# Performance work log

Hardware: AMD Instinct MI355X
Metric: run time of the kernel (lower is better)

The kernel has to match this reference:

```python
import jax, jax.numpy as jnp
import numpy as np

H = 300          # node_hidden_dim (GINE output dim)
D = 2 * H        # set2set in_channels = 600
STEPS = 2        # num_step_set2_set


def _lstm_cell(x, h, c, W_ih, W_hh, b_ih, b_hh):
    # PyTorch LSTM gate order: i, f, g, o
    gates = x @ W_ih.T + h @ W_hh.T + b_ih + b_hh
    i, f, g, o = jnp.split(gates, 4, axis=-1)
    c = jax.nn.sigmoid(f) * c + jax.nn.sigmoid(i) * jnp.tanh(g)
    h = jax.nn.sigmoid(o) * jnp.tanh(c)
    return h, c


def _set2set(x, batch, num_graphs, W_ih, W_hh, b_ih, b_hh):
    # torch_geometric Set2Set with processing_steps=STEPS, 1-layer LSTM
    B = num_graphs
    q_star = jnp.zeros((B, 2 * D), x.dtype)
    h = jnp.zeros((B, D), x.dtype)
    c = jnp.zeros((B, D), x.dtype)
    for _ in range(STEPS):
        h, c = _lstm_cell(q_star, h, c, W_ih, W_hh, b_ih, b_hh)
        q = h                                   # [B, D]
        e = jnp.sum(x * q[batch], axis=-1)      # [N]
        emax = jax.ops.segment_max(e, batch, num_segments=B)
        a = jnp.exp(e - emax[batch])
        asum = jax.ops.segment_sum(a, batch, num_segments=B)
        a = a / (asum[batch] + 1e-16)           # segment softmax
        r = jax.ops.segment_sum(a[:, None] * x, batch, num_segments=B)
        q_star = jnp.concatenate([q, r], axis=-1)   # [B, 2D]
    return q_star


def _l2norm(x):
    return x / jnp.maximum(jnp.linalg.norm(x, axis=1, keepdims=True), 1e-12)


def setup_inputs() -> dict:
    key = jax.random.key(0)
    ks = jax.random.split(key, 8)
    Nu, Nv, B = 8192, 8192, 256
    solute_x = jax.random.normal(ks[0], (Nu, H), jnp.float32)
    solvent_x = jax.random.normal(ks[1], (Nv, H), jnp.float32)
    solute_batch = jnp.sort(jax.random.randint(ks[2], (Nu,), 0, B)).astype(jnp.int32)
    solvent_batch = jnp.sort(jax.random.randint(ks[3], (Nv,), 0, B)).astype(jnp.int32)
    lstm_W_ih = jax.random.normal(ks[4], (4 * D, 2 * D), jnp.float32) * 0.02
    lstm_W_hh = jax.random.normal(ks[5], (4 * D, D), jnp.float32) * 0.02
    lstm_b_ih = jnp.zeros((4 * D,), jnp.float32)
    lstm_b_hh = jnp.zeros((4 * D,), jnp.float32)
    pred_W = jax.random.normal(ks[6], (1, 8 * H), jnp.float32) * 0.02
    pred_b = jnp.zeros((1,), jnp.float32)
    return {
        "solute_x": solute_x, "solvent_x": solvent_x,
        "solute_batch": solute_batch, "solvent_batch": solvent_batch,
        "num_graphs": B,
        "lstm_W_ih": lstm_W_ih, "lstm_W_hh": lstm_W_hh,
        "lstm_b_ih": lstm_b_ih, "lstm_b_hh": lstm_b_hh,
        "pred_W": pred_W, "pred_b": pred_b,
    }


def reference(solute_x, solvent_x, solute_batch, solvent_batch, num_graphs,
              lstm_W_ih, lstm_W_hh, lstm_b_ih, lstm_b_hh, pred_W, pred_b):
    # F.normalize(dim=1)
    su = _l2norm(solute_x)    # [Nu, H]
    sv = _l2norm(solvent_x)   # [Nv, H]
    # len_map = solute_len.T @ solvent_len == same-pair membership mask
    mask = (solute_batch[:, None] == solvent_batch[None, :]).astype(su.dtype)
    interaction_map = (su @ sv.T) * mask          # [Nu, Nv]
    ret_interaction_map = interaction_map
    solvent_prime = interaction_map.T @ su        # [Nv, H]
    solute_prime = interaction_map @ sv           # [Nu, H]
    su2 = jnp.concatenate([su, solute_prime], axis=1)    # [Nu, 2H]
    sv2 = jnp.concatenate([sv, solvent_prime], axis=1)   # [Nv, 2H]
    su_s2s = _set2set(su2, solute_batch, num_graphs, lstm_W_ih, lstm_W_hh, lstm_b_ih, lstm_b_hh)
    sv_s2s = _set2set(sv2, solvent_batch, num_graphs, lstm_W_ih, lstm_W_hh, lstm_b_ih, lstm_b_hh)
    final = jnp.concatenate([su_s2s, sv_s2s], axis=1)    # [B, 8H]
    predictions = final @ pred_W.T + pred_b              # [B, 1]
    return predictions, ret_interaction_map
```

## Files before the change

kernel.cpp:

```cpp
#include <hip/hip_runtime.h>
#include <math.h>

#define HDIM 300
#define DDIM 600
#define NGR  256

typedef float vf4 __attribute__((ext_vector_type(4)));
typedef float vf2 __attribute__((ext_vector_type(2)));

__device__ __forceinline__ float wred_sum(float v){
  #pragma unroll
  for(int o=32;o;o>>=1) v += __shfl_xor(v,o,64);
  return v;
}
__device__ __forceinline__ float wred_max(float v){
  #pragma unroll
  for(int o=32;o;o>>=1) v = fmaxf(v,__shfl_xor(v,o,64));
  return v;
}
__device__ __forceinline__ float sigm(float x){ return 1.f/(1.f+expf(-x)); }

__global__ __launch_bounds__(256) void k_norm_fill_off(const float* __restrict__ xu,
    const float* __restrict__ xv, float* __restrict__ su, float* __restrict__ sv,
    int Nu, int Nv, const int* __restrict__ ub, const int* __restrict__ vb,
    int* __restrict__ uoff, int* __restrict__ voff,
    const float* __restrict__ b_ih, const float* __restrict__ b_hh,
    float* __restrict__ h1, float* __restrict__ c1,
    const float* __restrict__ pb, float* __restrict__ outp,
    float* __restrict__ mapbase){
  int NBn = (Nu + Nv) >> 2;
  int b = blockIdx.x;
  if (b == NBn){
    int t = threadIdx.x;
    if (t < NGR){
      int lo=0, hi=Nu;
      while(lo<hi){ int m=(lo+hi)>>1; if (ub[m] < t) lo=m+1; else hi=m; }
      uoff[t]=lo;
      lo=0; hi=Nv;
      while(lo<hi){ int m=(lo+hi)>>1; if (vb[m] < t) lo=m+1; else hi=m; }
      voff[t]=lo;
      if (t==0){ uoff[NGR]=Nu; voff[NGR]=Nv; }
      outp[t] = pb[0];
    }
    for (int d=threadIdx.x; d<DDIM; d+=256){
      float gi = b_ih[d]      + b_hh[d];
      float gg = b_ih[1200+d] + b_hh[1200+d];
      float go = b_ih[1800+d] + b_hh[1800+d];
      float c  = sigm(gi)*tanhf(gg);
      c1[d]=c; h1[d]=sigm(go)*tanhf(c);
    }
    return;
  }
  if (b > NBn){
    int i = b - NBn - 1;
    int g = ub[i];
    int lo=0, hi=Nv;
    while(lo<hi){ int m=(lo+hi)>>1; if (vb[m] < g) lo=m+1; else hi=m; }
    int js = lo;
    hi = Nv;
    while(lo<hi){ int m=(lo+hi)>>1; if (vb[m] <= g) lo=m+1; else hi=m; }
    int je = lo;
    float* mrow = mapbase + (size_t)i*Nv;
    const vf4 z4 = {0.f,0.f,0.f,0.f};
    int nf4 = Nv >> 2;
    for (int q4=threadIdx.x; q4<nf4; q4+=256){
      int j0 = q4*4;
      if (j0+4 <= js || j0 >= je){
        __builtin_nontemporal_store(z4, (vf4*)(mrow + j0));
      } else {
        #pragma unroll
        for(int u=0;u<4;u++){ int j=j0+u; if (j<js || j>=je) mrow[j]=0.f; }
      }
    }
    return;
  }
  int wid = b*4 + (threadIdx.x >> 6);
  int lane = threadIdx.x & 63;
  const float* src; float* dst;
  if (wid < Nu){ src = xu + (size_t)wid*HDIM; dst = su + (size_t)wid*HDIM; }
  else         { src = xv + (size_t)(wid-Nu)*HDIM; dst = sv + (size_t)(wid-Nu)*HDIM; }
  const vf4* s4 = (const vf4*)src;
  vf4 A = s4[lane];
  vf4 Bv = (lane<11)? s4[64+lane] : (vf4){0.f,0.f,0.f,0.f};
  float s = A.x*A.x+A.y*A.y+A.z*A.z+A.w*A.w + Bv.x*Bv.x+Bv.y*Bv.y+Bv.z*Bv.z+Bv.w*Bv.w;
  s = wred_sum(s);
  float inv = 1.f / fmaxf(sqrtf(s), 1e-12f);
  vf4* d4 = (vf4*)dst;
  d4[lane] = A*inv;
  if (lane<11) d4[64+lane] = Bv*inv;
}

__global__ __launch_bounds__(256) void k_prime(const float* __restrict__ su,
    const float* __restrict__ sv, const int* __restrict__ ub,
    const int* __restrict__ vb, const int* __restrict__ uoff,
    const int* __restrict__ voff, float* __restrict__ spr,
    float* __restrict__ svp, float* __restrict__ e1u, float* __restrict__ e1v,
    const float* __restrict__ h1, float* __restrict__ mapbase, int Nu, int Nv){
  int b = blockIdx.x;
  bool isU = (b < Nu);
  int i = isU ? b : b - Nu;
  const float* xa = isU ? su : sv;
  const float* xb = isU ? sv : su;
  const int* mybatch = isU ? ub : vb;
  const int* ooff    = isU ? voff : uoff;
  float* prime = isU ? spr : svp;
  float* eout  = isU ? e1u : e1v;

  int tid = threadIdx.x, lane = tid & 63, w = tid >> 6;
  __shared__ __align__(16) float xrow[304];
  __shared__ __align__(16) float prl[4*304];
  __shared__ float qv[2*HDIM];
  __shared__ float red[4];
  const float* rowp = xa + (size_t)i*HDIM;
  for (int t=tid; t<HDIM;   t+=256) xrow[t] = rowp[t];
  for (int t=tid; t<2*HDIM; t+=256) qv[t]   = h1[t];
  int g = mybatch[i];
  int js = ooff[g], je = ooff[g+1];
  __syncthreads();

  const vf4* x4 = (const vf4*)xrow;
  vf4 xA = x4[lane];
  vf4 xB = (lane<11)? x4[64+lane] : (vf4){0.f,0.f,0.f,0.f};
  vf4 prA = {0.f,0.f,0.f,0.f}, prB = {0.f,0.f,0.f,0.f};
  for (int j = js + w; j < je; j += 4){
    const vf4* orow = (const vf4*)(xb + (size_t)j*HDIM);
    vf4 oA = orow[lane];
    vf4 oB = (lane<11)? orow[64+lane] : (vf4){0.f,0.f,0.f,0.f};
    float d = oA.x*xA.x + oA.y*xA.y + oA.z*xA.z + oA.w*xA.w
            + oB.x*xB.x + oB.y*xB.y + oB.z*xB.z + oB.w*xB.w;
    d = wred_sum(d);
    if (isU && lane==0) mapbase[(size_t)i*Nv + j] = d;
    prA += d * oA;
    prB += d * oB;
  }
  vf4* p4 = (vf4*)(prl + w*304);
  p4[lane] = prA;
  if (lane<11) p4[64+lane] = prB;
  __syncthreads();
  float ep = 0.f;
  for (int t=tid; t<HDIM; t+=256){
    float s = prl[t] + prl[304+t] + prl[608+t] + prl[912+t];
    prime[(size_t)i*HDIM + t] = s;
    ep += xrow[t]*qv[t] + s*qv[HDIM+t];
  }
  ep = wred_sum(ep);
  if (lane==0) red[w] = ep;
  __syncthreads();
  if (tid==0) eout[i] = red[0]+red[1]+red[2]+red[3];
}

__global__ __launch_bounds__(256) void k_r1_gbase(const float* __restrict__ su,
    const float* __restrict__ sv, const float* __restrict__ spr,
    const float* __restrict__ svp, const float* __restrict__ e1u,
    const float* __restrict__ e1v, const int* __restrict__ uoff,
    const int* __restrict__ voff, float* __restrict__ r1,
    const float* __restrict__ h1, const float* __restrict__ Wih,
    const float* __restrict__ Whh, const float* __restrict__ b_ih,
    const float* __restrict__ b_hh, float* __restrict__ gbase){
  int tid = threadIdx.x, lane = tid & 63, w = tid >> 6;
  if (blockIdx.x >= 512){
    int n = (blockIdx.x - 512)*4 + w;
    if (n >= 2400) return;
    const float* wi = Wih + (size_t)n*1200;
    const float* wh = Whh + (size_t)n*600;
    float s = 0.f;
    for (int k=lane; k<DDIM; k+=64) s += h1[k]*(wi[k] + wh[k]);
    s = wred_sum(s);
    if (lane==0) gbase[n] = s + b_ih[n] + b_hh[n];
    return;
  }
  int bs = blockIdx.x; int set = bs >> 8; int g = bs & 255;
  const float* x  = set? sv  : su;
  const float* pr = set? svp : spr;
  const float* e  = set? e1v : e1u;
  const int* off  = set? voff: uoff;
  __shared__ float al[2048]; __shared__ float red[4]; __shared__ float shv;
  int ns = off[g], ne = off[g+1]; int n = ne - ns;
  float m = -INFINITY;
  for (int t=ns+tid; t<ne; t+=256) m = fmaxf(m, e[t]);
  m = wred_max(m);
  if (lane==0) red[w]=m;
  __syncthreads();
  if (tid==0) shv = fmaxf(fmaxf(red[0],red[1]),fmaxf(red[2],red[3]));
  __syncthreads();
  float emax = shv;
  float s = 0.f;
  for (int t=tid; t<n; t+=256){ float a = expf(e[ns+t]-emax); if (t<2048) al[t]=a; s += a; }
  s = wred_sum(s);
  __syncthreads();
  if (lane==0) red[w]=s;
  __syncthreads();
  if (tid==0) shv = red[0]+red[1]+red[2]+red[3];
  __syncthreads();
  float inv = 1.f/(shv + 1e-16f);
  float acc[3] = {0.f,0.f,0.f};
  for (int nn=0; nn<n; nn++){
    float a = (nn<2048)? al[nn] : expf(e[ns+nn]-emax);
    const float* xr = x  + (size_t)(ns+nn)*HDIM;
    const float* pp = pr + (size_t)(ns+nn)*HDIM;
    #pragma unroll
    for(int u=0;u<3;u++){ int c = tid + u*256; if (c<DDIM){
        float xv = (c<HDIM)? xr[c] : pp[c-HDIM]; acc[u] += a*xv; } }
  }
  #pragma unroll
  for(int u=0;u<3;u++){ int c = tid + u*256; if (c<DDIM) r1[(size_t)bs*DDIM + c] = acc[u]*inv; }
}

__global__ __launch_bounds__(256) void k_gemm_lstm(const float* __restrict__ r1,
    const float* __restrict__ Wih, const float* __restrict__ gbase,
    const float* __restrict__ c1, float* __restrict__ h2){
  __shared__ __align__(16) float smem[32*68];
  float* Al = smem;
  float* Bl = smem + 16*36;
  int tid = threadIdx.x;
  int d0  = blockIdx.x*16;
  int gs0 = blockIdx.y*32;
  int tx = tid & 15, ty = tid >> 4;
  float acc[2][4] = {};
  for (int kt=0; kt<600; kt+=16){
    int k = kt + tx;
    bool kok = (k < 600);
    #pragma unroll
    for (int u=0; u<2; u++){
      int rl = ty + u*16;
      Al[tx*36 + rl] = kok ? r1[(size_t)(gs0+rl)*DDIM + k] : 0.f;
    }
    #pragma unroll
    for (int u=0; u<4; u++){
      int cl = ty + u*16;
      int gate = cl >> 4, dd = cl & 15;
      int d = d0 + dd;
      Bl[tx*68 + cl] = (kok && d < 600)
          ? Wih[(size_t)(gate*600 + d)*1200 + 600 + k] : 0.f;
    }
    __syncthreads();
    #pragma unroll
    for (int kk=0; kk<16; kk++){
      vf2 av = ((const vf2*)(Al + kk*36))[ty];
      vf4 bv = ((const vf4*)(Bl + kk*68))[tx];
      float a[2]={av.x,av.y}, bb[4]={bv.x,bv.y,bv.z,bv.w};
      #pragma unroll
      for(int mm=0;mm<2;mm++)
        #pragma unroll
        for(int nn=0;nn<4;nn++) acc[mm][nn] += a[mm]*bb[nn];
    }
    __syncthreads();
  }
  #pragma unroll
  for (int mm=0; mm<2; mm++){
    vf4 o = {acc[mm][0], acc[mm][1], acc[mm][2], acc[mm][3]};
    ((vf4*)(smem + (ty*2+mm)*68))[tx] = o;
  }
  __syncthreads();
  int d_l = tid & 15, r0 = tid >> 4;
  int d = d0 + d_l;
  if (d < 600){
    float gb_i = gbase[d], gb_f = gbase[600+d], gb_g = gbase[1200+d], gb_o = gbase[1800+d];
    float cc1 = c1[d];
    #pragma unroll
    for (int u=0; u<2; u++){
      int rl = r0 + u*16;
      const float* gr = smem + rl*68;
      float gi = gr[d_l]      + gb_i;
      float gf = gr[16+d_l]   + gb_f;
      float gG = gr[32+d_l]   + gb_g;
      float go = gr[48+d_l]   + gb_o;
      float c  = sigm(gf)*cc1 + sigm(gi)*tanhf(gG);
      h2[(size_t)(gs0+rl)*DDIM + d] = sigm(go)*tanhf(c);
    }
  }
}

__global__ __launch_bounds__(256) void k_r2(const float* __restrict__ su,
    const float* __restrict__ sv, const float* __restrict__ spr,
    const float* __restrict__ svp, const int* __restrict__ uoff,
    const int* __restrict__ voff, const float* __restrict__ h2,
    const float* __restrict__ pW, float* __restrict__ e2u,
    float* __restrict__ e2v, float* __restrict__ outp){
  int bs = blockIdx.x; int set = bs >> 8; int g = bs & 255;
  const float* x  = set? sv  : su;
  const float* pr = set? svp : spr;
  const int* off  = set? voff: uoff;
  float* e2       = set? e2v : e2u;
  int tid = threadIdx.x, lane = tid & 63, w = tid >> 6;
  __shared__ float q[DDIM]; __shared__ float al[2048];
  __shared__ float red[4]; __shared__ float shv;
  for (int t=tid; t<DDIM; t+=256) q[t] = h2[(size_t)bs*DDIM + t];
  int ns = off[g], ne = off[g+1]; int n = ne - ns;
  __syncthreads();
  for (int node = ns + w; node < ne; node += 4){
    const float* xr = x  + (size_t)node*HDIM;
    const float* pp = pr + (size_t)node*HDIM;
    float d = 0.f;
    #pragma unroll
    for(int c=0;c<10;c++){ int k = lane + 64*c; if (k<DDIM){
        float xv = (k<HDIM)? xr[k] : pp[k-HDIM]; d += xv*q[k]; } }
    d = wred_sum(d);
    if (lane==0) e2[node] = d;
  }
  __syncthreads();
  float m = -INFINITY;
  for (int t=ns+tid; t<ne; t+=256) m = fmaxf(m, e2[t]);
  m = wred_max(m);
  if (lane==0) red[w]=m;
  __syncthreads();
  if (tid==0) shv = fmaxf(fmaxf(red[0],red[1]),fmaxf(red[2],red[3]));
  __syncthreads();
  float emax = shv;
  float s = 0.f;
  for (int t=tid; t<n; t+=256){ float a = expf(e2[ns+t]-emax); if (t<2048) al[t]=a; s += a; }
  s = wred_sum(s);
  __syncthreads();
  if (lane==0) red[w]=s;
  __syncthreads();
  if (tid==0) shv = red[0]+red[1]+red[2]+red[3];
  __syncthreads();
  float inv = 1.f/(shv + 1e-16f);
  float acc[3] = {0.f,0.f,0.f};
  for (int nn=0; nn<n; nn++){
    float a = (nn<2048)? al[nn] : expf(e2[ns+nn]-emax);
    const float* xr = x  + (size_t)(ns+nn)*HDIM;
    const float* pp = pr + (size_t)(ns+nn)*HDIM;
    #pragma unroll
    for(int u=0;u<3;u++){ int c = tid + u*256; if (c<DDIM){
        float xv = (c<HDIM)? xr[c] : pp[c-HDIM]; acc[u] += a*xv; } }
  }
  int hoff = set? 1200 : 0;
  float p = 0.f;
  #pragma unroll
  for(int u=0;u<3;u++){ int c = tid + u*256; if (c<DDIM) p += (acc[u]*inv)*pW[hoff+600+c]; }
  for (int t=tid; t<DDIM; t+=256) p += q[t]*pW[hoff+t];
  p = wred_sum(p);
  __syncthreads();
  if (lane==0) red[w] = p;
  __syncthreads();
  if (tid==0) atomicAdd(&outp[g], red[0]+red[1]+red[2]+red[3]);
}

extern "C" void kernel_launch(void* const* d_in, const int* in_sizes, int n_in,
                              void* d_out, int out_size, void* d_ws, size_t ws_size,
                              hipStream_t stream) {
  const float* solute_x  = (const float*)d_in[0];
  const float* solvent_x = (const float*)d_in[1];
  const int*   ub        = (const int*)d_in[2];
  const int*   vb        = (const int*)d_in[3];
  const float* Wih  = (const float*)d_in[5];
  const float* Whh  = (const float*)d_in[6];
  const float* b_ih = (const float*)d_in[7];
  const float* b_hh = (const float*)d_in[8];
  const float* pW   = (const float*)d_in[9];
  const float* pb   = (const float*)d_in[10];

  int Nu = in_sizes[0] / HDIM;
  int Nv = in_sizes[1] / HDIM;

  float* out = (float*)d_out;
  int predn = out_size - Nu*Nv;
  float* mapbase = out + predn;

  float* ws = (float*)d_ws;
  float* su    = ws;
  float* sv    = su    + (size_t)Nu*HDIM;
  float* spr   = sv    + (size_t)Nv*HDIM;
  float* svp   = spr   + (size_t)Nu*HDIM;
  float* e1u   = svp   + (size_t)Nv*HDIM;
  float* e1v   = e1u   + Nu;
  float* h1    = e1v   + Nv;
  float* c1    = h1    + DDIM;
  float* r1    = c1    + DDIM;
  float* gbase = r1    + 512*DDIM;
  float* h2    = gbase + 2400;
  int*   uoff  = (int*)(h2 + 512*DDIM);
  int*   voff  = uoff + 257;

  int NBn = (Nu + Nv) / 4;
  k_norm_fill_off<<<dim3(NBn + 1 + Nu), dim3(256), 0, stream>>>(
      solute_x, solvent_x, su, sv, Nu, Nv, ub, vb, uoff, voff,
      b_ih, b_hh, h1, c1, pb, out, mapbase);
  k_prime<<<dim3(Nu+Nv), dim3(256), 0, stream>>>(
      su, sv, ub, vb, uoff, voff, spr, svp, e1u, e1v, h1, mapbase, Nu, Nv);
  k_r1_gbase<<<dim3(512+600), dim3(256), 0, stream>>>(
      su, sv, spr, svp, e1u, e1v, uoff, voff, r1, h1, Wih, Whh, b_ih, b_hh, gbase);
  k_gemm_lstm<<<dim3(38, 16), dim3(256), 0, stream>>>(r1, Wih, gbase, c1, h2);
  k_r2<<<dim3(512), dim3(256), 0, stream>>>(
      su, sv, spr, svp, uoff, voff, h2, pW, e1u, e1v, out);
}
```

Baseline: 548.6 us.

## Spread interaction-map zero fill across later kernels to overlap with compute

The zero-fill of the large Nu×Nv interaction map is moved out of the normalize kernel and split across k_prime (4096 rows), k_r1 (2048 rows) and k_r2 (2048 rows), running as extra blocks beside compute blocks. The gate-base GEMV also moves from k_r1 into k_prime. Row bounds now come from the precomputed voff table rather than per-block binary searches. The aim is to hide the write-bandwidth-bound fill behind latency-bound small kernels, at the cost of more blocks competing for those kernels' resources.

```diff
diff --git a/kernel.cpp b/kernel.cpp
--- a/kernel.cpp
+++ b/kernel.cpp
@@ -20,17 +20,32 @@
 }
 __device__ __forceinline__ float sigm(float x){ return 1.f/(1.f+expf(-x)); }
 
-__global__ __launch_bounds__(256) void k_norm_fill_off(const float* __restrict__ xu,
+__device__ __forceinline__ void fill_row(int i, const int* __restrict__ ub,
+    const int* __restrict__ voff, float* __restrict__ mapbase, int Nv, int tid){
+  int g = ub[i];
+  int js = voff[g], je = voff[g+1];
+  float* mrow = mapbase + (size_t)i*Nv;
+  const vf4 z4 = {0.f,0.f,0.f,0.f};
+  int nf4 = Nv >> 2;
+  for (int q4=tid; q4<nf4; q4+=256){
+    int j0 = q4*4;
+    if (j0+4 <= js || j0 >= je){
+      __builtin_nontemporal_store(z4, (vf4*)(mrow + j0));
+    } else {
+      #pragma unroll
+      for(int u=0;u<4;u++){ int j=j0+u; if (j<js || j>=je) mrow[j]=0.f; }
+    }
+  }
+}
+
+__global__ __launch_bounds__(256) void k_norm_off(const float* __restrict__ xu,
     const float* __restrict__ xv, float* __restrict__ su, float* __restrict__ sv,
     int Nu, int Nv, const int* __restrict__ ub, const int* __restrict__ vb,
     int* __restrict__ uoff, int* __restrict__ voff,
     const float* __restrict__ b_ih, const float* __restrict__ b_hh,
     float* __restrict__ h1, float* __restrict__ c1,
-    const float* __restrict__ pb, float* __restrict__ outp,
-    float* __restrict__ mapbase){
-  int NBn = (Nu + Nv) >> 2;
-  int b = blockIdx.x;
-  if (b == NBn){
+    const float* __restrict__ pb, float* __restrict__ outp){
+  if (blockIdx.x == gridDim.x - 1){
     int t = threadIdx.x;
     if (t < NGR){
       int lo=0, hi=Nu;
@@ -51,30 +66,7 @@
     }
     return;
   }
-  if (b > NBn){
-    int i = b - NBn - 1;
-    int g = ub[i];
-    int lo=0, hi=Nv;
-    while(lo<hi){ int m=(lo+hi)>>1; if (vb[m] < g) lo=m+1; else hi=m; }
-    int js = lo;
-    hi = Nv;
-    while(lo<hi){ int m=(lo+hi)>>1; if (vb[m] <= g) lo=m+1; else hi=m; }
-    int je = lo;
-    float* mrow = mapbase + (size_t)i*Nv;
-    const vf4 z4 = {0.f,0.f,0.f,0.f};
-    int nf4 = Nv >> 2;
-    for (int q4=threadIdx.x; q4<nf4; q4+=256){
-      int j0 = q4*4;
-      if (j0+4 <= js || j0 >= je){
-        __builtin_nontemporal_store(z4, (vf4*)(mrow + j0));
-      } else {
-        #pragma unroll
-        for(int u=0;u<4;u++){ int j=j0+u; if (j<js || j>=je) mrow[j]=0.f; }
-      }
-    }
-    return;
-  }
-  int wid = b*4 + (threadIdx.x >> 6);
+  int wid = blockIdx.x*4 + (threadIdx.x >> 6);
   int lane = threadIdx.x & 63;
   const float* src; float* dst;
   if (wid < Nu){ src = xu + (size_t)wid*HDIM; dst = su + (size_t)wid*HDIM; }
@@ -95,8 +87,27 @@
     const int* __restrict__ vb, const int* __restrict__ uoff,
     const int* __restrict__ voff, float* __restrict__ spr,
     float* __restrict__ svp, float* __restrict__ e1u, float* __restrict__ e1v,
-    const float* __restrict__ h1, float* __restrict__ mapbase, int Nu, int Nv){
+    const float* __restrict__ h1, float* __restrict__ mapbase, int Nu, int Nv,
+    const float* __restrict__ Wih, const float* __restrict__ Whh,
+    const float* __restrict__ b_ih, const float* __restrict__ b_hh,
+    float* __restrict__ gbase){
   int b = blockIdx.x;
+  int tid = threadIdx.x, lane = tid & 63, w = tid >> 6;
+  if (b >= Nu + Nv){
+    int e = b - (Nu + Nv);
+    if (e < 600){
+      int n = e*4 + w;
+      const float* wi = Wih + (size_t)n*1200;
+      const float* wh = Whh + (size_t)n*600;
+      float s = 0.f;
+      for (int k=lane; k<DDIM; k+=64) s += h1[k]*(wi[k] + wh[k]);
+      s = wred_sum(s);
+      if (lane==0) gbase[n] = s + b_ih[n] + b_hh[n];
+    } else {
+      fill_row(e - 600, ub, voff, mapbase, Nv, tid);
+    }
+    return;
+  }
   bool isU = (b < Nu);
   int i = isU ? b : b - Nu;
   const float* xa = isU ? su : sv;
@@ -106,7 +117,6 @@
   float* prime = isU ? spr : svp;
   float* eout  = isU ? e1u : e1v;
 
-  int tid = threadIdx.x, lane = tid & 63, w = tid >> 6;
   __shared__ __align__(16) float xrow[304];
   __shared__ __align__(16) float prl[4*304];
   __shared__ float qv[2*HDIM];
@@ -149,24 +159,15 @@
   if (tid==0) eout[i] = red[0]+red[1]+red[2]+red[3];
 }
 
-__global__ __launch_bounds__(256) void k_r1_gbase(const float* __restrict__ su,
+__global__ __launch_bounds__(256) void k_r1(const float* __restrict__ su,
     const float* __restrict__ sv, const float* __restrict__ spr,
     const float* __restrict__ svp, const float* __restrict__ e1u,
     const float* __restrict__ e1v, const int* __restrict__ uoff,
     const int* __restrict__ voff, float* __restrict__ r1,
-    const float* __restrict__ h1, const float* __restrict__ Wih,
-    const float* __restrict__ Whh, const float* __restrict__ b_ih,
-    const float* __restrict__ b_hh, float* __restrict__ gbase){
+    const int* __restrict__ ub, float* __restrict__ mapbase, int Nv){
   int tid = threadIdx.x, lane = tid & 63, w = tid >> 6;
   if (blockIdx.x >= 512){
-    int n = (blockIdx.x - 512)*4 + w;
-    if (n >= 2400) return;
-    const float* wi = Wih + (size_t)n*1200;
-    const float* wh = Whh + (size_t)n*600;
-    float s = 0.f;
-    for (int k=lane; k<DDIM; k+=64) s += h1[k]*(wi[k] + wh[k]);
-    s = wred_sum(s);
-    if (lane==0) gbase[n] = s + b_ih[n] + b_hh[n];
+    fill_row(4096 + (blockIdx.x - 512), ub, voff, mapbase, Nv, tid);
     return;
   }
   int bs = blockIdx.x; int set = bs >> 8; int g = bs & 255;
@@ -276,13 +277,18 @@
     const float* __restrict__ svp, const int* __restrict__ uoff,
     const int* __restrict__ voff, const float* __restrict__ h2,
     const float* __restrict__ pW, float* __restrict__ e2u,
-    float* __restrict__ e2v, float* __restrict__ outp){
+    float* __restrict__ e2v, float* __restrict__ outp,
+    const int* __restrict__ ub, float* __restrict__ mapbase, int Nv){
+  int tid = threadIdx.x, lane = tid & 63, w = tid >> 6;
+  if (blockIdx.x >= 512){
+    fill_row(6144 + (blockIdx.x - 512), ub, voff, mapbase, Nv, tid);
+    return;
+  }
   int bs = blockIdx.x; int set = bs >> 8; int g = bs & 255;
   const float* x  = set? sv  : su;
   const float* pr = set? svp : spr;
   const int* off  = set? voff: uoff;
   float* e2       = set? e2v : e2u;
-  int tid = threadIdx.x, lane = tid & 63, w = tid >> 6;
   __shared__ float q[DDIM]; __shared__ float al[2048];
   __shared__ float red[4]; __shared__ float shv;
   for (int t=tid; t<DDIM; t+=256) q[t] = h2[(size_t)bs*DDIM + t];
@@ -373,15 +379,15 @@
   int*   uoff  = (int*)(h2 + 512*DDIM);
   int*   voff  = uoff + 257;
 
-  int NBn = (Nu + Nv) / 4;
-  k_norm_fill_off<<<dim3(NBn + 1 + Nu), dim3(256), 0, stream>>>(
+  k_norm_off<<<dim3((Nu+Nv)/4 + 1), dim3(256), 0, stream>>>(
       solute_x, solvent_x, su, sv, Nu, Nv, ub, vb, uoff, voff,
-      b_ih, b_hh, h1, c1, pb, out, mapbase);
-  k_prime<<<dim3(Nu+Nv), dim3(256), 0, stream>>>(
-      su, sv, ub, vb, uoff, voff, spr, svp, e1u, e1v, h1, mapbase, Nu, Nv);
-  k_r1_gbase<<<dim3(512+600), dim3(256), 0, stream>>>(
-      su, sv, spr, svp, e1u, e1v, uoff, voff, r1, h1, Wih, Whh, b_ih, b_hh, gbase);
+      b_ih, b_hh, h1, c1, pb, out);
+  k_prime<<<dim3(Nu+Nv + 600 + 4096), dim3(256), 0, stream>>>(
+      su, sv, ub, vb, uoff, voff, spr, svp, e1u, e1v, h1, mapbase, Nu, Nv,
+      Wih, Whh, b_ih, b_hh, gbase);
+  k_r1<<<dim3(512 + 2048), dim3(256), 0, stream>>>(
+      su, sv, spr, svp, e1u, e1v, uoff, voff, r1, ub, mapbase, Nv);
   k_gemm_lstm<<<dim3(38, 16), dim3(256), 0, stream>>>(r1, Wih, gbase, c1, h2);
-  k_r2<<<dim3(512), dim3(256), 0, stream>>>(
-      su, sv, spr, svp, uoff, voff, h2, pW, e1u, e1v, out);
-}
+  k_r2<<<dim3(512 + 2048), dim3(256), 0, stream>>>(
+      su, sv, spr, svp, uoff, voff, h2, pW, e1u, e1v, out, ub, mapbase, Nv);
+}
```

Measured after the change: 535.0 us. 1.03x faster.

## Move interaction-map zero fill into prime kernel and gate base into norm kernel

Applied to the files above, without the earlier changes.

The zero fill of the large Nu×Nv interaction map moves from the first kernel into k_prime, interleaved with the prime rows (every third block fills a map row), and it now uses the precomputed voff offsets instead of binary searches. The LSTM gate-base GEMV moves from k_r1 into the first kernel, recomputing h1 locally in shared memory. The aim is to overlap the bandwidth-bound map write with the compute-bound prime work and to shorten the first and third kernels. k_r2 also shrinks its shared softmax buffer to 128 entries and spills larger segments to global memory, which may raise occupancy.

```diff
diff --git a/kernel.cpp b/kernel.cpp
--- a/kernel.cpp
+++ b/kernel.cpp
@@ -20,18 +20,38 @@
 }
 __device__ __forceinline__ float sigm(float x){ return 1.f/(1.f+expf(-x)); }
 
-__global__ __launch_bounds__(256) void k_norm_fill_off(const float* __restrict__ xu,
+__device__ __forceinline__ void fill_row(int i, const int* __restrict__ ub,
+    const int* __restrict__ voff, float* __restrict__ mapbase, int Nv, int tid){
+  int g = ub[i];
+  int js = voff[g], je = voff[g+1];
+  float* mrow = mapbase + (size_t)i*Nv;
+  const vf4 z4 = {0.f,0.f,0.f,0.f};
+  int nf4 = Nv >> 2;
+  for (int q4=tid; q4<nf4; q4+=256){
+    int j0 = q4*4;
+    if (j0+4 <= js || j0 >= je){
+      __builtin_nontemporal_store(z4, (vf4*)(mrow + j0));
+    } else {
+      #pragma unroll
+      for(int u=0;u<4;u++){ int j=j0+u; if (j<js || j>=je) mrow[j]=0.f; }
+    }
+  }
+}
+
+__global__ __launch_bounds__(256) void k_norm_off(const float* __restrict__ xu,
     const float* __restrict__ xv, float* __restrict__ su, float* __restrict__ sv,
     int Nu, int Nv, const int* __restrict__ ub, const int* __restrict__ vb,
     int* __restrict__ uoff, int* __restrict__ voff,
     const float* __restrict__ b_ih, const float* __restrict__ b_hh,
     float* __restrict__ h1, float* __restrict__ c1,
     const float* __restrict__ pb, float* __restrict__ outp,
-    float* __restrict__ mapbase){
+    const float* __restrict__ Wih, const float* __restrict__ Whh,
+    float* __restrict__ gbase){
   int NBn = (Nu + Nv) >> 2;
   int b = blockIdx.x;
+  int tid = threadIdx.x, lane = tid & 63, w = tid >> 6;
   if (b == NBn){
-    int t = threadIdx.x;
+    int t = tid;
     if (t < NGR){
       int lo=0, hi=Nu;
       while(lo<hi){ int m=(lo+hi)>>1; if (ub[m] < t) lo=m+1; else hi=m; }
@@ -42,7 +62,7 @@
       if (t==0){ uoff[NGR]=Nu; voff[NGR]=Nv; }
       outp[t] = pb[0];
     }
-    for (int d=threadIdx.x; d<DDIM; d+=256){
+    for (int d=tid; d<DDIM; d+=256){
       float gi = b_ih[d]      + b_hh[d];
       float gg = b_ih[1200+d] + b_hh[1200+d];
       float go = b_ih[1800+d] + b_hh[1800+d];
@@ -52,30 +72,25 @@
     return;
   }
   if (b > NBn){
-    int i = b - NBn - 1;
-    int g = ub[i];
-    int lo=0, hi=Nv;
-    while(lo<hi){ int m=(lo+hi)>>1; if (vb[m] < g) lo=m+1; else hi=m; }
-    int js = lo;
-    hi = Nv;
-    while(lo<hi){ int m=(lo+hi)>>1; if (vb[m] <= g) lo=m+1; else hi=m; }
-    int je = lo;
-    float* mrow = mapbase + (size_t)i*Nv;
-    const vf4 z4 = {0.f,0.f,0.f,0.f};
-    int nf4 = Nv >> 2;
-    for (int q4=threadIdx.x; q4<nf4; q4+=256){
-      int j0 = q4*4;
-      if (j0+4 <= js || j0 >= je){
-        __builtin_nontemporal_store(z4, (vf4*)(mrow + j0));
-      } else {
-        #pragma unroll
-        for(int u=0;u<4;u++){ int j=j0+u; if (j<js || j>=je) mrow[j]=0.f; }
-      }
-    }
+    __shared__ float h1l[DDIM];
+    for (int d=tid; d<DDIM; d+=256){
+      float gi = b_ih[d]      + b_hh[d];
+      float gg = b_ih[1200+d] + b_hh[1200+d];
+      float go = b_ih[1800+d] + b_hh[1800+d];
+      float c  = sigm(gi)*tanhf(gg);
+      h1l[d]   = sigm(go)*tanhf(c);
+    }
+    __syncthreads();
+    int n = (b - NBn - 1)*4 + w;
+    const float* wi = Wih + (size_t)n*1200;
+    const float* wh = Whh + (size_t)n*600;
+    float s = 0.f;
+    for (int k=lane; k<DDIM; k+=64) s += h1l[k]*(wi[k] + wh[k]);
+    s = wred_sum(s);
+    if (lane==0) gbase[n] = s + b_ih[n] + b_hh[n];
     return;
   }
-  int wid = b*4 + (threadIdx.x >> 6);
-  int lane = threadIdx.x & 63;
+  int wid = b*4 + w;
   const float* src; float* dst;
   if (wid < Nu){ src = xu + (size_t)wid*HDIM; dst = su + (size_t)wid*HDIM; }
   else         { src = xv + (size_t)(wid-Nu)*HDIM; dst = sv + (size_t)(wid-Nu)*HDIM; }
@@ -97,8 +112,12 @@
     float* __restrict__ svp, float* __restrict__ e1u, float* __restrict__ e1v,
     const float* __restrict__ h1, float* __restrict__ mapbase, int Nu, int Nv){
   int b = blockIdx.x;
-  bool isU = (b < Nu);
-  int i = isU ? b : b - Nu;
+  int tid = threadIdx.x, lane = tid & 63, w = tid >> 6;
+  int r = b % 3;
+  if (r == 2){ fill_row(b/3, ub, voff, mapbase, Nv, tid); return; }
+  int idx = (b/3)*2 + r;
+  bool isU = (idx < Nu);
+  int i = isU ? idx : idx - Nu;
   const float* xa = isU ? su : sv;
   const float* xb = isU ? sv : su;
   const int* mybatch = isU ? ub : vb;
@@ -106,7 +125,6 @@
   float* prime = isU ? spr : svp;
   float* eout  = isU ? e1u : e1v;
 
-  int tid = threadIdx.x, lane = tid & 63, w = tid >> 6;
   __shared__ __align__(16) float xrow[304];
   __shared__ __align__(16) float prl[4*304];
   __shared__ float qv[2*HDIM];
@@ -149,26 +167,12 @@
   if (tid==0) eout[i] = red[0]+red[1]+red[2]+red[3];
 }
 
-__global__ __launch_bounds__(256) void k_r1_gbase(const float* __restrict__ su,
+__global__ __launch_bounds__(256) void k_r1(const float* __restrict__ su,
     const float* __restrict__ sv, const float* __restrict__ spr,
     const float* __restrict__ svp, const float* __restrict__ e1u,
     const float* __restrict__ e1v, const int* __restrict__ uoff,
-    const int* __restrict__ voff, float* __restrict__ r1,
-    const float* __restrict__ h1, const float* __restrict__ Wih,
-    const float* __restrict__ Whh, const float* __restrict__ b_ih,
-    const float* __restrict__ b_hh, float* __restrict__ gbase){
+    const int* __restrict__ voff, float* __restrict__ r1){
   int tid = threadIdx.x, lane = tid & 63, w = tid >> 6;
-  if (blockIdx.x >= 512){
-    int n = (blockIdx.x - 512)*4 + w;
-    if (n >= 2400) return;
-    const float* wi = Wih + (size_t)n*1200;
-    const float* wh = Whh + (size_t)n*600;
-    float s = 0.f;
-    for (int k=lane; k<DDIM; k+=64) s += h1[k]*(wi[k] + wh[k]);
-    s = wred_sum(s);
-    if (lane==0) gbase[n] = s + b_ih[n] + b_hh[n];
-    return;
-  }
   int bs = blockIdx.x; int set = bs >> 8; int g = bs & 255;
   const float* x  = set? sv  : su;
   const float* pr = set? svp : spr;
@@ -277,13 +281,13 @@
     const int* __restrict__ voff, const float* __restrict__ h2,
     const float* __restrict__ pW, float* __restrict__ e2u,
     float* __restrict__ e2v, float* __restrict__ outp){
+  int tid = threadIdx.x, lane = tid & 63, w = tid >> 6;
   int bs = blockIdx.x; int set = bs >> 8; int g = bs & 255;
   const float* x  = set? sv  : su;
   const float* pr = set? svp : spr;
   const int* off  = set? voff: uoff;
-  float* e2       = set? e2v : e2u;
-  int tid = threadIdx.x, lane = tid & 63, w = tid >> 6;
-  __shared__ float q[DDIM]; __shared__ float al[2048];
+  float* e2g      = set? e2v : e2u;
+  __shared__ float q[DDIM]; __shared__ float e2l[128]; __shared__ float al[128];
   __shared__ float red[4]; __shared__ float shv;
   for (int t=tid; t<DDIM; t+=256) q[t] = h2[(size_t)bs*DDIM + t];
   int ns = off[g], ne = off[g+1]; int n = ne - ns;
@@ -296,11 +300,11 @@
     for(int c=0;c<10;c++){ int k = lane + 64*c; if (k<DDIM){
         float xv = (k<HDIM)? xr[k] : pp[k-HDIM]; d += xv*q[k]; } }
     d = wred_sum(d);
-    if (lane==0) e2[node] = d;
+    if (lane==0){ int t = node-ns; if (t<128) e2l[t] = d; else e2g[node] = d; }
   }
   __syncthreads();
   float m = -INFINITY;
-  for (int t=ns+tid; t<ne; t+=256) m = fmaxf(m, e2[t]);
+  for (int t=tid; t<n; t+=256) m = fmaxf(m, (t<128)? e2l[t] : e2g[ns+t]);
   m = wred_max(m);
   if (lane==0) red[w]=m;
   __syncthreads();
@@ -308,7 +312,11 @@
   __syncthreads();
   float emax = shv;
   float s = 0.f;
-  for (int t=tid; t<n; t+=256){ float a = expf(e2[ns+t]-emax); if (t<2048) al[t]=a; s += a; }
+  for (int t=tid; t<n; t+=256){
+    float a = expf(((t<128)? e2l[t] : e2g[ns+t]) - emax);
+    if (t<128) al[t]=a; else e2g[ns+t]=a;
+    s += a;
+  }
   s = wred_sum(s);
   __syncthreads();
   if (lane==0) red[w]=s;
@@ -318,7 +326,7 @@
   float inv = 1.f/(shv + 1e-16f);
   float acc[3] = {0.f,0.f,0.f};
   for (int nn=0; nn<n; nn++){
-    float a = (nn<2048)? al[nn] : expf(e2[ns+nn]-emax);
+    float a = (nn<128)? al[nn] : e2g[ns+nn];
     const float* xr = x  + (size_t)(ns+nn)*HDIM;
     const float* pp = pr + (size_t)(ns+nn)*HDIM;
     #pragma unroll
@@ -373,14 +381,13 @@
   int*   uoff  = (int*)(h2 + 512*DDIM);
   int*   voff  = uoff + 257;
 
-  int NBn = (Nu + Nv) / 4;
-  k_norm_fill_off<<<dim3(NBn + 1 + Nu), dim3(256), 0, stream>>>(
+  k_norm_off<<<dim3((Nu+Nv)/4 + 1 + 600), dim3(256), 0, stream>>>(
       solute_x, solvent_x, su, sv, Nu, Nv, ub, vb, uoff, voff,
-      b_ih, b_hh, h1, c1, pb, out, mapbase);
-  k_prime<<<dim3(Nu+Nv), dim3(256), 0, stream>>>(
+      b_ih, b_hh, h1, c1, pb, out, Wih, Whh, gbase);
+  k_prime<<<dim3(24576), dim3(256), 0, stream>>>(
       su, sv, ub, vb, uoff, voff, spr, svp, e1u, e1v, h1, mapbase, Nu, Nv);
-  k_r1_gbase<<<dim3(512+600), dim3(256), 0, stream>>>(
-      su, sv, spr, svp, e1u, e1v, uoff, voff, r1, h1, Wih, Whh, b_ih, b_hh, gbase);
+  k_r1<<<dim3(512), dim3(256), 0, stream>>>(
+      su, sv, spr, svp, e1u, e1v, uoff, voff, r1);
   k_gemm_lstm<<<dim3(38, 16), dim3(256), 0, stream>>>(r1, Wih, gbase, c1, h2);
   k_r2<<<dim3(512), dim3(256), 0, stream>>>(
       su, sv, spr, svp, uoff, voff, h2, pW, e1u, e1v, out);
```

Measured after the change: 524.6 us. -4.4%, faster.
